# Performance work log

Hardware: AMD Instinct MI355X
Metric: run time of the kernel (lower is better)

The kernel has to match this reference:

```python
import jax, jax.numpy as jnp
import numpy as np

GRID_SIZE = 8
IN_DIM = 1024
OUT_DIM = 1024
BATCH = 4096


def setup_inputs() -> dict:
    key = jax.random.key(0)
    k1, k2, k3 = jax.random.split(key, 3)
    noise_scale = 0.1
    noise_scale_base = 0.1
    x = jax.random.normal(k1, (BATCH, IN_DIM), dtype=jnp.float32)
    scale_base = (1.0 / np.sqrt(IN_DIM)
                  + (jax.random.normal(k2, (OUT_DIM, IN_DIM), dtype=jnp.float32) * 2 - 1)
                  * noise_scale_base)
    scale_spline = jnp.full((OUT_DIM, IN_DIM), 1.0, dtype=jnp.float32)
    coeff = (jax.random.uniform(k3, (2, OUT_DIM, IN_DIM, GRID_SIZE), dtype=jnp.float32)
             * noise_scale / (np.sqrt(IN_DIM) * np.sqrt(GRID_SIZE)))
    return {"x": x, "scale_base": scale_base, "scale_spline": scale_spline,
            "coeff": coeff}


def reference(x, scale_base, scale_spline, coeff):
    # x: (B, I); scale_base/scale_spline: (O, I); coeff: (2, O, I, G)
    G = coeff.shape[-1]
    k = jnp.arange(1, G + 1, dtype=x.dtype)          # (G,)
    ang = x[:, :, None] * k                           # (B, I, G)
    cos_b = jnp.cos(ang)
    sin_b = jnp.sin(ang)
    # fold scale_spline into coeff: (2, O, I, G)
    w = scale_spline[None, :, :, None] * coeff
    spline = (jnp.einsum('big,oig->bo', cos_b, w[0])
              + jnp.einsum('big,oig->bo', sin_b, w[1]))  # (B, O)
    base = jnp.einsum('bi,oi->bo', jax.nn.silu(x), scale_base)
    return base + spline
```

## Files before the change

### kernel.cpp

```cpp
#include <hip/hip_runtime.h>
#include <hip/hip_bf16.h>
#include <stdint.h>

#define BATCH   4096
#define IN_DIM  1024
#define OUT_DIM 1024
#define GRID_G  8
#define K8      16384
#define KB      1024
#define SPLITK  2
#define WSCALE  256.0f

typedef __bf16 bf16x8 __attribute__((ext_vector_type(8)));
typedef __bf16 bf16x4 __attribute__((ext_vector_type(4)));
typedef float  f32x4  __attribute__((ext_vector_type(4)));
typedef int    i32x4  __attribute__((ext_vector_type(4)));
typedef int    i32x8  __attribute__((ext_vector_type(8)));

__global__ __launch_bounds__(256) void prep(const float* __restrict__ x,
                                            const float* __restrict__ sb,
                                            const float* __restrict__ ss,
                                            const float* __restrict__ coeff,
                                            uint8_t* __restrict__ A8,
                                            uint8_t* __restrict__ W8,
                                            __bf16* __restrict__ Ab,
                                            __bf16* __restrict__ Wb,
                                            float* __restrict__ C) {
    __shared__ __align__(16) float lds[8192];
    const int tid = threadIdx.x;

    if (blockIdx.x < 1024) {
        const int t  = blockIdx.x * 256 + tid;
        const int b  = t >> 6;
        const int i0 = (t & 63) * 16;

        {
            float4 z = make_float4(0.f, 0.f, 0.f, 0.f);
            float4* cz = (float4*)(C + (size_t)blockIdx.x * 4096);
#pragma unroll
            for (int j = 0; j < 4; ++j) cz[j * 256 + tid] = z;
        }

        float xv[16];
        {
            const f32x4* xp = (const f32x4*)(x + (size_t)b * IN_DIM + i0);
            f32x4 q0 = __builtin_nontemporal_load(xp + 0);
            f32x4 q1 = __builtin_nontemporal_load(xp + 1);
            f32x4 q2 = __builtin_nontemporal_load(xp + 2);
            f32x4 q3 = __builtin_nontemporal_load(xp + 3);
#pragma unroll
            for (int j = 0; j < 4; ++j) {
                xv[j]      = q0[j];
                xv[4 + j]  = q1[j];
                xv[8 + j]  = q2[j];
                xv[12 + j] = q3[j];
            }
        }

        float c1[16], s1[16], ck[16], sk[16];
        bf16x8 va, vb;
#pragma unroll
        for (int j = 0; j < 16; ++j) {
            float e  = __expf(-xv[j]);
            float sl = xv[j] * __builtin_amdgcn_rcpf(1.f + e);
            if (j < 8) va[j & 7] = (__bf16)sl; else vb[j & 7] = (__bf16)sl;
            s1[j] = __sinf(xv[j]);
            c1[j] = __cosf(xv[j]);
            ck[j] = c1[j]; sk[j] = s1[j];
        }
        __builtin_nontemporal_store(va, (bf16x8*)(Ab + (size_t)b * IN_DIM + i0));
        __builtin_nontemporal_store(vb, (bf16x8*)(Ab + (size_t)b * IN_DIM + i0 + 8));

        uint8_t* a8 = A8 + (size_t)b * K8 + i0;
#pragma unroll
        for (int g = 0; g < GRID_G; ++g) {
            i32x4 wc, ws;
#pragma unroll
            for (int q = 0; q < 4; ++q) {
                int dc = 0, ds = 0;
                dc = __builtin_amdgcn_cvt_pk_fp8_f32(ck[4*q+0], ck[4*q+1], dc, false);
                dc = __builtin_amdgcn_cvt_pk_fp8_f32(ck[4*q+2], ck[4*q+3], dc, true);
                ds = __builtin_amdgcn_cvt_pk_fp8_f32(sk[4*q+0], sk[4*q+1], ds, false);
                ds = __builtin_amdgcn_cvt_pk_fp8_f32(sk[4*q+2], sk[4*q+3], ds, true);
                wc[q] = dc; ws[q] = ds;
            }
            __builtin_nontemporal_store(wc, (i32x4*)(a8 + (size_t)g * IN_DIM));
            __builtin_nontemporal_store(ws, (i32x4*)(a8 + (size_t)(GRID_G + g) * IN_DIM));
            if (g < GRID_G - 1) {
#pragma unroll
                for (int j = 0; j < 16; ++j) {
                    float cn = ck[j] * c1[j] - sk[j] * s1[j];
                    float sn = sk[j] * c1[j] + ck[j] * s1[j];
                    ck[j] = cn; sk[j] = sn;
                }
            }
        }
    } else {
        const int o   = blockIdx.x - 1024;
        const int i0  = tid * 4;
        const size_t oi = (size_t)o * IN_DIM + i0;

        const f32x4 s4 = __builtin_nontemporal_load((const f32x4*)(ss + oi));
        const float  s[4] = {s4[0] * WSCALE, s4[1] * WSCALE, s4[2] * WSCALE, s4[3] * WSCALE};

        {
            f32x4 b4 = __builtin_nontemporal_load((const f32x4*)(sb + oi));
            bf16x4 wv;
            wv[0] = (__bf16)b4[0]; wv[1] = (__bf16)b4[1];
            wv[2] = (__bf16)b4[2]; wv[3] = (__bf16)b4[3];
            __builtin_nontemporal_store(wv, (bf16x4*)(Wb + oi));
        }

        uint8_t* w8 = W8 + (size_t)o * K8 + i0;
        for (int p = 0; p < 2; ++p) {
            if (p) __syncthreads();
            const f32x4* src = (const f32x4*)(coeff + ((size_t)p * OUT_DIM + o) * (IN_DIM * GRID_G));
#pragma unroll
            for (int j = 0; j < 8; ++j) {
                f32x4 v = __builtin_nontemporal_load(src + j * 256 + tid);
                const int L   = j * 4096 + tid * 16;
                const int row = L >> 7;
                const int ch  = (L >> 4) & 7;
                *(f32x4*)((uint8_t*)lds + row * 128 + ((ch ^ (row & 7)) << 4)) = v;
            }
            __syncthreads();
            float c[4][8];
            {
                const uint8_t* rp = (const uint8_t*)lds + tid * 128;
                const int r7 = (tid & 7) << 4;
#pragma unroll
                for (int j = 0; j < 8; ++j) {
                    f32x4 v = *(const f32x4*)(rp + ((j << 4) ^ r7));
                    c[j >> 1][(j & 1) * 4 + 0] = v[0];
                    c[j >> 1][(j & 1) * 4 + 1] = v[1];
                    c[j >> 1][(j & 1) * 4 + 2] = v[2];
                    c[j >> 1][(j & 1) * 4 + 3] = v[3];
                }
            }
#pragma unroll
            for (int g = 0; g < GRID_G; ++g) {
                int d = 0;
                d = __builtin_amdgcn_cvt_pk_fp8_f32(s[0]*c[0][g], s[1]*c[1][g], d, false);
                d = __builtin_amdgcn_cvt_pk_fp8_f32(s[2]*c[2][g], s[3]*c[3][g], d, true);
                __builtin_nontemporal_store(d, (int*)(w8 + (size_t)(p * GRID_G + g) * IN_DIM));
            }
        }
    }
}

__global__ __launch_bounds__(256, 2) void gemm_all(const uint8_t* __restrict__ A8,
                                                   const uint8_t* __restrict__ W8,
                                                   const uint8_t* __restrict__ Ab,
                                                   const uint8_t* __restrict__ Wb,
                                                   float* __restrict__ C) {
    __shared__ __align__(16) uint8_t As[2][16384];
    __shared__ __align__(16) uint8_t Bs[2][16384];
    const int tid = threadIdx.x;
    const int w   = tid >> 6;
    const int l   = tid & 63;
    const int flat = blockIdx.y * 8 + blockIdx.x;
    const int xcd  = flat & 7;
    const int idx  = flat >> 3;
    const int bn   = (xcd & 1) * 4 + (idx & 3);
    const int bm   = (xcd >> 1) * 8 + (idx >> 2);
    const int kz  = blockIdx.z;
    const int wm  = w & 1;
    const int wn  = w >> 1;

    f32x4 acc[4][4] = {};

    const int srow   = l >> 3;
    const int schunk = ((l & 7) ^ srow) * 16;
    const int lm = l & 15;
    const int q  = l >> 4;
    const int c0 = (q * 2) << 4, c1 = (q * 2 + 1) << 4;

    {
        const uint8_t* Ag = A8 + (size_t)(bm * 128 + w * 32 + srow) * K8 + kz * (K8 / SPLITK) + schunk;
        const uint8_t* Bg = W8 + (size_t)(bn * 128 + w * 32 + srow) * K8 + kz * (K8 / SPLITK) + schunk;

        auto stage = [&](int bb) {
#pragma unroll
            for (int j = 0; j < 4; ++j) {
                __builtin_amdgcn_global_load_lds(
                    (const uint32_t*)(Ag + (size_t)(j * 8) * K8),
                    (uint32_t*)(&As[bb][(w * 32 + j * 8) * 128]), 16, 0, 0);
                __builtin_amdgcn_global_load_lds(
                    (const uint32_t*)(Bg + (size_t)(j * 8) * K8),
                    (uint32_t*)(&Bs[bb][(w * 32 + j * 8) * 128]), 16, 0, 0);
            }
            Ag += 128; Bg += 128;
        };
        auto compute = [&](int bb) {
            i32x8 bf[4];
#pragma unroll
            for (int j = 0; j < 4; ++j) {
                const int row = wn * 64 + j * 16 + lm;
                const int sw  = (row & 7) << 4;
                const uint8_t* rp = &Bs[bb][row * 128];
                i32x4 lo = *(const i32x4*)(rp + (c0 ^ sw));
                i32x4 hi = *(const i32x4*)(rp + (c1 ^ sw));
                bf[j] = __builtin_shufflevector(lo, hi, 0, 1, 2, 3, 4, 5, 6, 7);
            }
#pragma unroll
            for (int i = 0; i < 4; ++i) {
                const int row = wm * 64 + i * 16 + lm;
                const int sw  = (row & 7) << 4;
                const uint8_t* rp = &As[bb][row * 128];
                i32x4 lo = *(const i32x4*)(rp + (c0 ^ sw));
                i32x4 hi = *(const i32x4*)(rp + (c1 ^ sw));
                i32x8 af = __builtin_shufflevector(lo, hi, 0, 1, 2, 3, 4, 5, 6, 7);
#pragma unroll
                for (int j = 0; j < 4; ++j)
                    acc[i][j] = __builtin_amdgcn_mfma_scale_f32_16x16x128_f8f6f4(
                        af, bf[j], acc[i][j], 0, 0, 0, 0x7f7f7f7f, 0, 0x7f7f7f7f);
            }
        };

        stage(0);
        stage(1);
        const int NT = (K8 / SPLITK) / 128;
        for (int t = 0; t < NT; ++t) {
            if (t < NT - 1) { asm volatile("s_waitcnt vmcnt(8)" ::: "memory"); }
            else            { asm volatile("s_waitcnt vmcnt(0)" ::: "memory"); }
            __builtin_amdgcn_sched_barrier(0);
            __builtin_amdgcn_s_barrier();
            compute(t & 1);
            __builtin_amdgcn_s_barrier();
            if (t < NT - 2) stage(t & 1);
        }
    }

#pragma unroll
    for (int i = 0; i < 4; ++i)
#pragma unroll
        for (int j = 0; j < 4; ++j)
            acc[i][j] *= (1.0f / WSCALE);

    {
        const uint8_t* Ag = Ab + (size_t)(bm * 128 + w * 32 + srow) * (KB * 2) + kz * (KB * 2 / SPLITK) + schunk;
        const uint8_t* Bg = Wb + (size_t)(bn * 128 + w * 32 + srow) * (KB * 2) + kz * (KB * 2 / SPLITK) + schunk;

        auto stage = [&](int bb) {
#pragma unroll
            for (int j = 0; j < 4; ++j) {
                __builtin_amdgcn_global_load_lds(
                    (const uint32_t*)(Ag + (size_t)(j * 8) * (KB * 2)),
                    (uint32_t*)(&As[bb][(w * 32 + j * 8) * 128]), 16, 0, 0);
                __builtin_amdgcn_global_load_lds(
                    (const uint32_t*)(Bg + (size_t)(j * 8) * (KB * 2)),
                    (uint32_t*)(&Bs[bb][(w * 32 + j * 8) * 128]), 16, 0, 0);
            }
            Ag += 128; Bg += 128;
        };
        auto compute = [&](int bb) {
#pragma unroll
            for (int h = 0; h < 2; ++h) {
                bf16x8 af[4], bfr[4];
#pragma unroll
                for (int i = 0; i < 4; ++i) {
                    const int row = wm * 64 + i * 16 + lm;
                    af[i] = *(const bf16x8*)(&As[bb][row * 128 + ((((h * 4 + q) ^ (row & 7))) << 4)]);
                }
#pragma unroll
                for (int j = 0; j < 4; ++j) {
                    const int row = wn * 64 + j * 16 + lm;
                    bfr[j] = *(const bf16x8*)(&Bs[bb][row * 128 + ((((h * 4 + q) ^ (row & 7))) << 4)]);
                }
#pragma unroll
                for (int i = 0; i < 4; ++i)
#pragma unroll
                    for (int j = 0; j < 4; ++j)
                        acc[i][j] = __builtin_amdgcn_mfma_f32_16x16x32_bf16(af[i], bfr[j], acc[i][j], 0, 0, 0);
            }
        };

        stage(0);
        stage(1);
        const int NT = (KB * 2 / SPLITK) / 128;
        for (int t = 0; t < NT; ++t) {
            if (t < NT - 1) { asm volatile("s_waitcnt vmcnt(8)" ::: "memory"); }
            else            { asm volatile("s_waitcnt vmcnt(0)" ::: "memory"); }
            __builtin_amdgcn_sched_barrier(0);
            __builtin_amdgcn_s_barrier();
            compute(t & 1);
            __builtin_amdgcn_s_barrier();
            if (t < NT - 2) stage(t & 1);
        }
    }

    const int row0 = bm * 128 + wm * 64 + q * 4;
    const int col0 = bn * 128 + wn * 64 + lm;
#pragma unroll
    for (int i = 0; i < 4; ++i)
#pragma unroll
        for (int j = 0; j < 4; ++j)
#pragma unroll
            for (int r = 0; r < 4; ++r)
                unsafeAtomicAdd(&C[(size_t)(row0 + i * 16 + r) * OUT_DIM + col0 + j * 16],
                                acc[i][j][r]);
}

extern "C" void kernel_launch(void* const* d_in, const int* in_sizes, int n_in,
                              void* d_out, int out_size, void* d_ws, size_t ws_size,
                              hipStream_t stream) {
    const float* x     = (const float*)d_in[0];
    const float* sb    = (const float*)d_in[1];
    const float* ss    = (const float*)d_in[2];
    const float* coeff = (const float*)d_in[3];
    float* out = (float*)d_out;

    uint8_t* A8 = (uint8_t*)d_ws;
    uint8_t* W8 = A8 + (size_t)BATCH * K8;
    __bf16*  Ab = (__bf16*)(W8 + (size_t)OUT_DIM * K8);
    __bf16*  Wb = Ab + (size_t)BATCH * KB;

    hipLaunchKernelGGL(prep, dim3(2048), dim3(256), 0, stream,
                       x, sb, ss, coeff, A8, W8, Ab, Wb, out);
    hipLaunchKernelGGL(gemm_all, dim3(OUT_DIM / 128, BATCH / 128, SPLITK), dim3(256), 0, stream,
                       A8, W8, (const uint8_t*)Ab, (const uint8_t*)Wb, out);
}
```

Before: 243.2 us.

## Generate fp8 Chebyshev harmonics inside GEMM from staged cos/sin table

The prep kernel no longer materialises the full 4096x16384 fp8 harmonic matrix. It writes only fp32 cos/sin pairs per (b,i), and the GEMM rebuilds harmonics 1..8 in LDS with a Chebyshev recurrence per K-tile: cosine for split 0, sine for split 1. The W8 layout moves to i-major with g innermost so it matches the generated A order, and prep's coeff path becomes a direct per-element load without the LDS transpose. This removes the large A8 write and reread in exchange for ALU work and extra barriers inside the GEMM main loop, a larger LDS footprint (80KB) that may hurt occupancy, and possible accumulation error from the recurrence.

```diff
diff --git a/kernel.cpp b/kernel.cpp
--- a/kernel.cpp
+++ b/kernel.cpp
@@ -9,24 +9,26 @@
 #define K8      16384
 #define KB      1024
 #define SPLITK  2
+#define TPITCH  8192
 #define WSCALE  256.0f
 
 typedef __bf16 bf16x8 __attribute__((ext_vector_type(8)));
 typedef __bf16 bf16x4 __attribute__((ext_vector_type(4)));
 typedef float  f32x4  __attribute__((ext_vector_type(4)));
+typedef int    i32x2  __attribute__((ext_vector_type(2)));
 typedef int    i32x4  __attribute__((ext_vector_type(4)));
 typedef int    i32x8  __attribute__((ext_vector_type(8)));
+
 
 __global__ __launch_bounds__(256) void prep(const float* __restrict__ x,
                                             const float* __restrict__ sb,
                                             const float* __restrict__ ss,
                                             const float* __restrict__ coeff,
-                                            uint8_t* __restrict__ A8,
+                                            uint8_t* __restrict__ T,
                                             uint8_t* __restrict__ W8,
                                             __bf16* __restrict__ Ab,
                                             __bf16* __restrict__ Wb,
                                             float* __restrict__ C) {
-    __shared__ __align__(16) float lds[8192];
     const int tid = threadIdx.x;
 
     if (blockIdx.x < 1024) {
@@ -50,14 +52,11 @@
             f32x4 q3 = __builtin_nontemporal_load(xp + 3);
 #pragma unroll
             for (int j = 0; j < 4; ++j) {
-                xv[j]      = q0[j];
-                xv[4 + j]  = q1[j];
-                xv[8 + j]  = q2[j];
-                xv[12 + j] = q3[j];
-            }
-        }
-
-        float c1[16], s1[16], ck[16], sk[16];
+                xv[j] = q0[j]; xv[4+j] = q1[j]; xv[8+j] = q2[j]; xv[12+j] = q3[j];
+            }
+        }
+
+        float c1[16], s1[16];
         bf16x8 va, vb;
 #pragma unroll
         for (int j = 0; j < 16; ++j) {
@@ -66,95 +65,56 @@
             if (j < 8) va[j & 7] = (__bf16)sl; else vb[j & 7] = (__bf16)sl;
             s1[j] = __sinf(xv[j]);
             c1[j] = __cosf(xv[j]);
-            ck[j] = c1[j]; sk[j] = s1[j];
         }
         __builtin_nontemporal_store(va, (bf16x8*)(Ab + (size_t)b * IN_DIM + i0));
         __builtin_nontemporal_store(vb, (bf16x8*)(Ab + (size_t)b * IN_DIM + i0 + 8));
 
-        uint8_t* a8 = A8 + (size_t)b * K8 + i0;
-#pragma unroll
-        for (int g = 0; g < GRID_G; ++g) {
-            i32x4 wc, ws;
-#pragma unroll
-            for (int q = 0; q < 4; ++q) {
-                int dc = 0, ds = 0;
-                dc = __builtin_amdgcn_cvt_pk_fp8_f32(ck[4*q+0], ck[4*q+1], dc, false);
-                dc = __builtin_amdgcn_cvt_pk_fp8_f32(ck[4*q+2], ck[4*q+3], dc, true);
-                ds = __builtin_amdgcn_cvt_pk_fp8_f32(sk[4*q+0], sk[4*q+1], ds, false);
-                ds = __builtin_amdgcn_cvt_pk_fp8_f32(sk[4*q+2], sk[4*q+3], ds, true);
-                wc[q] = dc; ws[q] = ds;
-            }
-            __builtin_nontemporal_store(wc, (i32x4*)(a8 + (size_t)g * IN_DIM));
-            __builtin_nontemporal_store(ws, (i32x4*)(a8 + (size_t)(GRID_G + g) * IN_DIM));
-            if (g < GRID_G - 1) {
-#pragma unroll
-                for (int j = 0; j < 16; ++j) {
-                    float cn = ck[j] * c1[j] - sk[j] * s1[j];
-                    float sn = sk[j] * c1[j] + ck[j] * s1[j];
-                    ck[j] = cn; sk[j] = sn;
-                }
-            }
+        uint8_t* tp = T + (size_t)b * TPITCH + (size_t)i0 * 8;
+#pragma unroll
+        for (int e2 = 0; e2 < 8; ++e2) {
+            f32x4 tv; tv[0] = c1[2*e2]; tv[1] = s1[2*e2]; tv[2] = c1[2*e2+1]; tv[3] = s1[2*e2+1];
+            __builtin_nontemporal_store(tv, (f32x4*)(tp + e2 * 16));
         }
     } else {
-        const int o   = blockIdx.x - 1024;
-        const int i0  = tid * 4;
-        const size_t oi = (size_t)o * IN_DIM + i0;
-
-        const f32x4 s4 = __builtin_nontemporal_load((const f32x4*)(ss + oi));
-        const float  s[4] = {s4[0] * WSCALE, s4[1] * WSCALE, s4[2] * WSCALE, s4[3] * WSCALE};
-
+        const int u = (blockIdx.x - 1024) * 256 + tid;
+        const int o = u >> 10;
+        const int i = u & 1023;
+        const size_t oi = (size_t)o * IN_DIM + i;
+
+        const float s = __builtin_nontemporal_load(ss + oi) * WSCALE;
         {
-            f32x4 b4 = __builtin_nontemporal_load((const f32x4*)(sb + oi));
-            bf16x4 wv;
-            wv[0] = (__bf16)b4[0]; wv[1] = (__bf16)b4[1];
-            wv[2] = (__bf16)b4[2]; wv[3] = (__bf16)b4[3];
-            __builtin_nontemporal_store(wv, (bf16x4*)(Wb + oi));
-        }
-
-        uint8_t* w8 = W8 + (size_t)o * K8 + i0;
+            float bv = __builtin_nontemporal_load(sb + oi);
+            Wb[oi] = (__bf16)bv;
+        }
+        uint8_t* w8 = W8 + (size_t)o * K8 + (size_t)i * 8;
+#pragma unroll
         for (int p = 0; p < 2; ++p) {
-            if (p) __syncthreads();
-            const f32x4* src = (const f32x4*)(coeff + ((size_t)p * OUT_DIM + o) * (IN_DIM * GRID_G));
-#pragma unroll
-            for (int j = 0; j < 8; ++j) {
-                f32x4 v = __builtin_nontemporal_load(src + j * 256 + tid);
-                const int L   = j * 4096 + tid * 16;
-                const int row = L >> 7;
-                const int ch  = (L >> 4) & 7;
-                *(f32x4*)((uint8_t*)lds + row * 128 + ((ch ^ (row & 7)) << 4)) = v;
-            }
-            __syncthreads();
-            float c[4][8];
-            {
-                const uint8_t* rp = (const uint8_t*)lds + tid * 128;
-                const int r7 = (tid & 7) << 4;
-#pragma unroll
-                for (int j = 0; j < 8; ++j) {
-                    f32x4 v = *(const f32x4*)(rp + ((j << 4) ^ r7));
-                    c[j >> 1][(j & 1) * 4 + 0] = v[0];
-                    c[j >> 1][(j & 1) * 4 + 1] = v[1];
-                    c[j >> 1][(j & 1) * 4 + 2] = v[2];
-                    c[j >> 1][(j & 1) * 4 + 3] = v[3];
-                }
-            }
-#pragma unroll
-            for (int g = 0; g < GRID_G; ++g) {
-                int d = 0;
-                d = __builtin_amdgcn_cvt_pk_fp8_f32(s[0]*c[0][g], s[1]*c[1][g], d, false);
-                d = __builtin_amdgcn_cvt_pk_fp8_f32(s[2]*c[2][g], s[3]*c[3][g], d, true);
-                __builtin_nontemporal_store(d, (int*)(w8 + (size_t)(p * GRID_G + g) * IN_DIM));
-            }
+            const f32x4* cp = (const f32x4*)(coeff + (((size_t)p * OUT_DIM + o) * IN_DIM + i) * GRID_G);
+            f32x4 a0 = __builtin_nontemporal_load(cp + 0);
+            f32x4 a1 = __builtin_nontemporal_load(cp + 1);
+            int d0 = 0, d1 = 0;
+            d0 = __builtin_amdgcn_cvt_pk_fp8_f32(s*a0[0], s*a0[1], d0, false);
+            d0 = __builtin_amdgcn_cvt_pk_fp8_f32(s*a0[2], s*a0[3], d0, true);
+            d1 = __builtin_amdgcn_cvt_pk_fp8_f32(s*a1[0], s*a1[1], d1, false);
+            d1 = __builtin_amdgcn_cvt_pk_fp8_f32(s*a1[2], s*a1[3], d1, true);
+            i32x2 dd; dd[0] = d0; dd[1] = d1;
+            __builtin_nontemporal_store(dd, (i32x2*)(w8 + (size_t)p * 8192));
         }
     }
 }
 
-__global__ __launch_bounds__(256, 2) void gemm_all(const uint8_t* __restrict__ A8,
+__global__ __launch_bounds__(256, 2) void gemm_all(const uint8_t* __restrict__ Tg_,
                                                    const uint8_t* __restrict__ W8,
                                                    const uint8_t* __restrict__ Ab,
                                                    const uint8_t* __restrict__ Wb,
                                                    float* __restrict__ C) {
-    __shared__ __align__(16) uint8_t As[2][16384];
-    __shared__ __align__(16) uint8_t Bs[2][16384];
+    __shared__ __align__(16) uint8_t pool[81920];
+    uint8_t* Abuf  = pool;
+    uint8_t* Bb0   = pool + 16384;
+    uint8_t* Bb1   = pool + 32768;
+    uint8_t* Tb0   = pool + 49152;
+    uint8_t* Tb1   = pool + 65536;
+
     const int tid = threadIdx.x;
     const int w   = tid >> 6;
     const int l   = tid & 63;
@@ -176,28 +136,68 @@
     const int c0 = (q * 2) << 4, c1 = (q * 2 + 1) << 4;
 
     {
-        const uint8_t* Ag = A8 + (size_t)(bm * 128 + w * 32 + srow) * K8 + kz * (K8 / SPLITK) + schunk;
-        const uint8_t* Bg = W8 + (size_t)(bn * 128 + w * 32 + srow) * K8 + kz * (K8 / SPLITK) + schunk;
-
-        auto stage = [&](int bb) {
-#pragma unroll
-            for (int j = 0; j < 4; ++j) {
+        const uint8_t* Tg = Tg_ + (size_t)(bm * 128 + w * 32 + srow) * TPITCH + schunk;
+        const uint8_t* Bg = W8 + (size_t)(bn * 128 + w * 32 + srow) * K8 + kz * 8192 + schunk;
+
+        auto stageT = [&](uint8_t* dst) {
+#pragma unroll
+            for (int j = 0; j < 4; ++j)
                 __builtin_amdgcn_global_load_lds(
-                    (const uint32_t*)(Ag + (size_t)(j * 8) * K8),
-                    (uint32_t*)(&As[bb][(w * 32 + j * 8) * 128]), 16, 0, 0);
+                    (const uint32_t*)(Tg + (size_t)(j * 8) * TPITCH),
+                    (uint32_t*)(dst + (w * 32 + j * 8) * 128), 16, 0, 0);
+            Tg += 128;
+        };
+        auto stageB = [&](uint8_t* dst) {
+#pragma unroll
+            for (int j = 0; j < 4; ++j)
                 __builtin_amdgcn_global_load_lds(
                     (const uint32_t*)(Bg + (size_t)(j * 8) * K8),
-                    (uint32_t*)(&Bs[bb][(w * 32 + j * 8) * 128]), 16, 0, 0);
-            }
-            Ag += 128; Bg += 128;
-        };
-        auto compute = [&](int bb) {
+                    (uint32_t*)(dst + (w * 32 + j * 8) * 128), 16, 0, 0);
+            Bg += 128;
+        };
+
+        const int r   = tid >> 1;
+        const int i8  = tid & 1;
+        const int key = r & 7;
+        auto agen = [&](const uint8_t* tsrc) {
+            const uint8_t* trow = tsrc + r * 128;
+            uint8_t*       arow = Abuf + r * 128;
+#pragma unroll
+            for (int c = 0; c < 4; ++c) {
+                const int ch = ((i8 * 4 + c) ^ key) << 4;
+                f32x4 tv = *(const f32x4*)(trow + ch);
+                i32x4 wv;
+#pragma unroll
+                for (int e = 0; e < 2; ++e) {
+                    float cc = tv[e * 2], sn = tv[e * 2 + 1];
+                    float tc = cc + cc;
+                    float g1, g2;
+                    if (kz == 0) { g1 = cc; g2 = tc * cc - 1.0f; }
+                    else         { g1 = sn; g2 = tc * sn; }
+                    float g3 = tc * g2 - g1;
+                    float g4 = tc * g3 - g2;
+                    float g5 = tc * g4 - g3;
+                    float g6 = tc * g5 - g4;
+                    float g7 = tc * g6 - g5;
+                    float g8 = tc * g7 - g6;
+                    int d0 = 0, d1 = 0;
+                    d0 = __builtin_amdgcn_cvt_pk_fp8_f32(g1, g2, d0, false);
+                    d0 = __builtin_amdgcn_cvt_pk_fp8_f32(g3, g4, d0, true);
+                    d1 = __builtin_amdgcn_cvt_pk_fp8_f32(g5, g6, d1, false);
+                    d1 = __builtin_amdgcn_cvt_pk_fp8_f32(g7, g8, d1, true);
+                    wv[e * 2] = d0; wv[e * 2 + 1] = d1;
+                }
+                *(i32x4*)(arow + ch) = wv;
+            }
+        };
+
+        auto mfma = [&](const uint8_t* bsrc) {
             i32x8 bf[4];
 #pragma unroll
             for (int j = 0; j < 4; ++j) {
                 const int row = wn * 64 + j * 16 + lm;
                 const int sw  = (row & 7) << 4;
-                const uint8_t* rp = &Bs[bb][row * 128];
+                const uint8_t* rp = bsrc + row * 128;
                 i32x4 lo = *(const i32x4*)(rp + (c0 ^ sw));
                 i32x4 hi = *(const i32x4*)(rp + (c1 ^ sw));
                 bf[j] = __builtin_shufflevector(lo, hi, 0, 1, 2, 3, 4, 5, 6, 7);
@@ -206,7 +206,7 @@
             for (int i = 0; i < 4; ++i) {
                 const int row = wm * 64 + i * 16 + lm;
                 const int sw  = (row & 7) << 4;
-                const uint8_t* rp = &As[bb][row * 128];
+                const uint8_t* rp = Abuf + row * 128;
                 i32x4 lo = *(const i32x4*)(rp + (c0 ^ sw));
                 i32x4 hi = *(const i32x4*)(rp + (c1 ^ sw));
                 i32x8 af = __builtin_shufflevector(lo, hi, 0, 1, 2, 3, 4, 5, 6, 7);
@@ -217,75 +217,92 @@
             }
         };
 
-        stage(0);
-        stage(1);
-        const int NT = (K8 / SPLITK) / 128;
+        stageT(Tb0); stageB(Bb0);
+        asm volatile("s_waitcnt vmcnt(0)" ::: "memory");
+        __builtin_amdgcn_sched_barrier(0);
+        __builtin_amdgcn_s_barrier();
+
+        for (int t = 0; t < 64; ++t) {
+            const int par = t & 1;
+            agen(par ? Tb1 : Tb0);
+            if (t < 63) { stageT(par ? Tb0 : Tb1); stageB(par ? Bb0 : Bb1); }
+            asm volatile("s_waitcnt lgkmcnt(0)" ::: "memory");
+            __builtin_amdgcn_sched_barrier(0);
+            if (t < 63) { asm volatile("s_waitcnt vmcnt(8)" ::: "memory"); }
+            else        { asm volatile("s_waitcnt vmcnt(0)" ::: "memory"); }
+            __builtin_amdgcn_sched_barrier(0);
+            __builtin_amdgcn_s_barrier();
+            mfma(par ? Bb1 : Bb0);
+            if (t < 63) {
+                asm volatile("s_waitcnt vmcnt(4)" ::: "memory");
+                __builtin_amdgcn_sched_barrier(0);
+                __builtin_amdgcn_s_barrier();
+            }
+        }
+    }
+
+#pragma unroll
+    for (int i = 0; i < 4; ++i)
+#pragma unroll
+        for (int j = 0; j < 4; ++j)
+            acc[i][j] *= (1.0f / WSCALE);
+
+    __syncthreads();
+
+    {
+        uint8_t* A0 = pool;
+        uint8_t* A1 = pool + 16384;
+        uint8_t* B0 = pool + 32768;
+        uint8_t* B1 = pool + 49152;
+        const uint8_t* Ag = Ab + (size_t)(bm * 128 + w * 32 + srow) * (KB * 2) + kz * (KB * 2 / SPLITK) + schunk;
+        const uint8_t* Bg = Wb + (size_t)(bn * 128 + w * 32 + srow) * (KB * 2) + kz * (KB * 2 / SPLITK) + schunk;
+
+        auto stage = [&](uint8_t* Ad, uint8_t* Bd) {
+#pragma unroll
+            for (int j = 0; j < 4; ++j) {
+                __builtin_amdgcn_global_load_lds(
+                    (const uint32_t*)(Ag + (size_t)(j * 8) * (KB * 2)),
+                    (uint32_t*)(Ad + (w * 32 + j * 8) * 128), 16, 0, 0);
+                __builtin_amdgcn_global_load_lds(
+                    (const uint32_t*)(Bg + (size_t)(j * 8) * (KB * 2)),
+                    (uint32_t*)(Bd + (w * 32 + j * 8) * 128), 16, 0, 0);
+            }
+            Ag += 128; Bg += 128;
+        };
+        auto compute = [&](const uint8_t* Asrc, const uint8_t* Bsrc) {
+#pragma unroll
+            for (int h = 0; h < 2; ++h) {
+                bf16x8 af[4], bfr[4];
+#pragma unroll
+                for (int i = 0; i < 4; ++i) {
+                    const int row = wm * 64 + i * 16 + lm;
+                    af[i] = *(const bf16x8*)(Asrc + row * 128 + ((((h * 4 + q) ^ (row & 7))) << 4));
+                }
+#pragma unroll
+                for (int j = 0; j < 4; ++j) {
+                    const int row = wn * 64 + j * 16 + lm;
+                    bfr[j] = *(const bf16x8*)(Bsrc + row * 128 + ((((h * 4 + q) ^ (row & 7))) << 4));
+                }
+#pragma unroll
+                for (int i = 0; i < 4; ++i)
+#pragma unroll
+                    for (int j = 0; j < 4; ++j)
+                        acc[i][j] = __builtin_amdgcn_mfma_f32_16x16x32_bf16(af[i], bfr[j], acc[i][j], 0, 0, 0);
+            }
+        };
+
+        stage(A0, B0);
+        stage(A1, B1);
+        const int NT = (KB * 2 / SPLITK) / 128;
         for (int t = 0; t < NT; ++t) {
+            const int par = t & 1;
             if (t < NT - 1) { asm volatile("s_waitcnt vmcnt(8)" ::: "memory"); }
             else            { asm volatile("s_waitcnt vmcnt(0)" ::: "memory"); }
             __builtin_amdgcn_sched_barrier(0);
             __builtin_amdgcn_s_barrier();
-            compute(t & 1);
+            compute(par ? A1 : A0, par ? B1 : B0);
             __builtin_amdgcn_s_barrier();
-            if (t < NT - 2) stage(t & 1);
-        }
-    }
-
-#pragma unroll
-    for (int i = 0; i < 4; ++i)
-#pragma unroll
-        for (int j = 0; j < 4; ++j)
-            acc[i][j] *= (1.0f / WSCALE);
-
-    {
-        const uint8_t* Ag = Ab + (size_t)(bm * 128 + w * 32 + srow) * (KB * 2) + kz * (KB * 2 / SPLITK) + schunk;
-        const uint8_t* Bg = Wb + (size_t)(bn * 128 + w * 32 + srow) * (KB * 2) + kz * (KB * 2 / SPLITK) + schunk;
-
-        auto stage = [&](int bb) {
-#pragma unroll
-            for (int j = 0; j < 4; ++j) {
-                __builtin_amdgcn_global_load_lds(
-                    (const uint32_t*)(Ag + (size_t)(j * 8) * (KB * 2)),
-                    (uint32_t*)(&As[bb][(w * 32 + j * 8) * 128]), 16, 0, 0);
-                __builtin_amdgcn_global_load_lds(
-                    (const uint32_t*)(Bg + (size_t)(j * 8) * (KB * 2)),
-                    (uint32_t*)(&Bs[bb][(w * 32 + j * 8) * 128]), 16, 0, 0);
-            }
-            Ag += 128; Bg += 128;
-        };
-        auto compute = [&](int bb) {
-#pragma unroll
-            for (int h = 0; h < 2; ++h) {
-                bf16x8 af[4], bfr[4];
-#pragma unroll
-                for (int i = 0; i < 4; ++i) {
-                    const int row = wm * 64 + i * 16 + lm;
-                    af[i] = *(const bf16x8*)(&As[bb][row * 128 + ((((h * 4 + q) ^ (row & 7))) << 4)]);
-                }
-#pragma unroll
-                for (int j = 0; j < 4; ++j) {
-                    const int row = wn * 64 + j * 16 + lm;
-                    bfr[j] = *(const bf16x8*)(&Bs[bb][row * 128 + ((((h * 4 + q) ^ (row & 7))) << 4)]);
-                }
-#pragma unroll
-                for (int i = 0; i < 4; ++i)
-#pragma unroll
-                    for (int j = 0; j < 4; ++j)
-                        acc[i][j] = __builtin_amdgcn_mfma_f32_16x16x32_bf16(af[i], bfr[j], acc[i][j], 0, 0, 0);
-            }
-        };
-
-        stage(0);
-        stage(1);
-        const int NT = (KB * 2 / SPLITK) / 128;
-        for (int t = 0; t < NT; ++t) {
-            if (t < NT - 1) { asm volatile("s_waitcnt vmcnt(8)" ::: "memory"); }
-            else            { asm volatile("s_waitcnt vmcnt(0)" ::: "memory"); }
-            __builtin_amdgcn_sched_barrier(0);
-            __builtin_amdgcn_s_barrier();
-            compute(t & 1);
-            __builtin_amdgcn_s_barrier();
-            if (t < NT - 2) stage(t & 1);
+            if (t < NT - 2) stage(par ? A1 : A0, par ? B1 : B0);
         }
     }
 
@@ -310,13 +327,13 @@
     const float* coeff = (const float*)d_in[3];
     float* out = (float*)d_out;
 
-    uint8_t* A8 = (uint8_t*)d_ws;
-    uint8_t* W8 = A8 + (size_t)BATCH * K8;
+    uint8_t* T  = (uint8_t*)d_ws;
+    uint8_t* W8 = T + (size_t)BATCH * TPITCH;
     __bf16*  Ab = (__bf16*)(W8 + (size_t)OUT_DIM * K8);
     __bf16*  Wb = Ab + (size_t)BATCH * KB;
 
-    hipLaunchKernelGGL(prep, dim3(2048), dim3(256), 0, stream,
-                       x, sb, ss, coeff, A8, W8, Ab, Wb, out);
+    hipLaunchKernelGGL(prep, dim3(1024 + 4096), dim3(256), 0, stream,
+                       x, sb, ss, coeff, T, W8, Ab, Wb, out);
     hipLaunchKernelGGL(gemm_all, dim3(OUT_DIM / 128, BATCH / 128, SPLITK), dim3(256), 0, stream,
-                       A8, W8, (const uint8_t*)Ab, (const uint8_t*)Wb, out);
+                       T, W8, (const uint8_t*)Ab, (const uint8_t*)Wb, out);
 }
```

Result: slower. 282.3 us (+16.1%).
